# Kernel optimization log

Hardware: AMD Instinct MI355X
Metric: run time of the kernel (lower is better)

The kernel has to match this reference:

```python
import jax, jax.numpy as jnp
import numpy as np

N_NODES = 100000
N_EDGES = 1600000
DIM_NODE = 128
DIM_HID = 128
N_CLASSES = 10


def gcn_conv(x, src, dst, W, b, num_nodes):
    # PyG GCNConv: h = W x; out[i] = sum_j norm_ij * h[j] + b, with self-loops
    # and symmetric normalization norm_ij = deg(i)^-1/2 * deg(j)^-1/2.
    ones = jnp.ones(src.shape[0], dtype=x.dtype)
    deg = jax.ops.segment_sum(ones, dst, num_segments=num_nodes)  # in-degree incl self-loop
    dinv = jnp.where(deg > 0, jax.lax.rsqrt(deg), 0.0)
    norm = dinv[src] * dinv[dst]                                  # [E+N]
    h = x @ W                                                     # [N, out]
    msg = h[src] * norm[:, None]                                  # gather + scale
    out = jax.ops.segment_sum(msg, dst, num_segments=num_nodes)   # scatter-add
    return out + b


def setup_inputs() -> dict:
    key = jax.random.key(0)
    ks = jax.random.split(key, 8)
    x = jax.random.normal(ks[0], (N_NODES, DIM_NODE), dtype=jnp.float32)
    edge_index = jax.random.randint(ks[1], (2, N_EDGES), 0, N_NODES, dtype=jnp.int32)
    def lin(k, fan_in, fan_out):
        s = 1.0 / np.sqrt(fan_in)
        return jax.random.uniform(k, (fan_in, fan_out), jnp.float32, -s, s)
    W1 = lin(ks[2], DIM_NODE, DIM_HID)
    W2 = lin(ks[3], DIM_HID, DIM_HID)
    W3 = lin(ks[4], DIM_HID, DIM_HID)
    fW1 = lin(ks[5], DIM_HID, DIM_HID)
    fW2 = lin(ks[6], DIM_HID, N_CLASSES)
    z = lambda n: jnp.zeros((n,), jnp.float32)
    return {"x": x, "edge_index": edge_index,
            "W1": W1, "b1": z(DIM_HID), "W2": W2, "b2": z(DIM_HID),
            "W3": W3, "b3": z(DIM_HID), "fW1": fW1, "fb1": z(DIM_HID),
            "fW2": fW2, "fb2": z(N_CLASSES)}


def reference(x, edge_index, W1, b1, W2, b2, W3, b3, fW1, fb1, fW2, fb2):
    num_nodes = x.shape[0]
    loop = jnp.arange(num_nodes, dtype=edge_index.dtype)
    src = jnp.concatenate([edge_index[0], loop])  # add self-loops once
    dst = jnp.concatenate([edge_index[1], loop])
    h = jax.nn.relu(gcn_conv(x, src, dst, W1, b1, num_nodes))
    h = jax.nn.relu(gcn_conv(h, src, dst, W2, b2, num_nodes))
    h = jax.nn.relu(gcn_conv(h, src, dst, W3, b3, num_nodes))
    # FFN head (Dropout is identity in eval mode)
    h = jax.nn.relu(h @ fW1 + fb1)
    out = h @ fW2 + fb2
    return out
```

## Files before the change

kernel.cpp:

```cpp
#include <hip/hip_runtime.h>
#include <hip/hip_bf16.h>
#include <hip/hip_fp16.h>

#define DIM 128
#define ROWS 16
#define NCAP 64
#define NSH  6
#define NXCD 8

typedef __attribute__((ext_vector_type(8))) short bf16x8;
typedef __attribute__((ext_vector_type(4))) float f32x4;
typedef _Float16 half_t;

union Frag { unsigned int u[4]; bf16x8 v; uint4 q; };
union H8   { uint4 q; half_t h[8]; };

__device__ __forceinline__ void cvt_hilo(const float* __restrict__ x, Frag& hi, Frag& lo) {
#pragma unroll
    for (int p = 0; p < 4; ++p) {
        float x0 = x[2 * p], x1 = x[2 * p + 1];
        unsigned int h0 = (__float_as_uint(x0) + 0x8000u) & 0xffff0000u;
        unsigned int h1 = (__float_as_uint(x1) + 0x8000u) & 0xffff0000u;
        hi.u[p] = (h0 >> 16) | h1;
        float d0 = x0 - __uint_as_float(h0);
        float d1 = x1 - __uint_as_float(h1);
        lo.u[p] = (__float_as_uint(d0) >> 16) | (__float_as_uint(d1) & 0xffff0000u);
    }
}

__global__ __launch_bounds__(256) void ncur_init_kernel(int* __restrict__ ncur, int N) {
    int n = blockIdx.x * 256 + threadIdx.x;
    if (n < N) ncur[n] = n << NSH;
}

__global__ __launch_bounds__(256) void scatter8_kernel(
    const int* __restrict__ src, const int* __restrict__ dst,
    int* __restrict__ ncur, int* __restrict__ colidx, int E, int N) {
    const int g    = blockIdx.x & (NXCD - 1);
    const int sub  = blockIdx.x >> 3;
    const int nsub = gridDim.x >> 3;
    const int slice = (N + NXCD - 1) / NXCD;
    const int lo = g * slice;
    const int hi = min(lo + slice, N);
    for (int e = sub * 256 + threadIdx.x; e < E; e += nsub * 256) {
        int d = dst[e];
        if (d >= lo && d < hi) {
            int p = atomicAdd(&ncur[d], 1);
            if (p < (d << NSH) + NCAP) colidx[p] = src[e];
        }
    }
}

__global__ __launch_bounds__(256) void ninfo_kernel(
    const int* __restrict__ ncur, unsigned int* __restrict__ ninfo,
    float* __restrict__ dinv, int N) {
    int n = blockIdx.x * 256 + threadIdx.x;
    if (n < N) {
        int deg = min(ncur[n] - (n << NSH), NCAP);
        ninfo[n] = (unsigned int)(n << NSH) | ((unsigned int)deg << 23);
        dinv[n]  = rsqrtf((float)(deg + 1));
    }
}

__global__ __launch_bounds__(256) void wconv_all_kernel(
    const float* __restrict__ W0, const float* __restrict__ W1,
    const float* __restrict__ W2, const float* __restrict__ W3,
    uint4* __restrict__ WFhi, uint4* __restrict__ WFlo) {
    int t  = blockIdx.x * 256 + threadIdx.x;
    int wi = t >> 11;
    const float* W = (wi == 0) ? W0 : (wi == 1) ? W1 : (wi == 2) ? W2 : W3;
    int tt   = t & 2047;
    int lane = tt & 63;
    int f    = tt >> 6;
    int kc   = f >> 3;
    int wc   = (f >> 2) & 1;
    int ct   = f & 3;
    int m    = lane & 15;
    int quad = lane >> 4;
    int col  = wc * 64 + ct * 16 + m;
    int k0   = kc * 32 + quad * 8;
    float wv8[8];
#pragma unroll
    for (int j = 0; j < 8; ++j) wv8[j] = W[(size_t)(k0 + j) * DIM + col];
    Frag hi, lo;
    cvt_hilo(wv8, hi, lo);
    WFhi[t] = hi.q;
    WFlo[t] = lo.q;
}

template<bool GATHER, bool FFN>
__global__ __launch_bounds__(256, 4) void fused16(
    const unsigned int* __restrict__ ninfo, const int* __restrict__ colidx,
    const void* __restrict__ HinV, const float* __restrict__ bg,
    const float* __restrict__ dinv,
    const uint4* __restrict__ WFhi, const uint4* __restrict__ WFlo,
    const float* __restrict__ fb1,
    const float* __restrict__ fW2, const float* __restrict__ fb2,
    void* __restrict__ YV, int N)
{
    __shared__ uint4 Sbuf[512];
    __shared__ float Wl[FFN ? (DIM * 10 + 16) : 1];

    const int tid  = threadIdx.x;
    const int row0 = blockIdx.x * ROWS;

    if constexpr (FFN) {
        for (int i = tid; i < DIM * 10; i += 256) Wl[i] = fW2[i];
        if (tid < 10) Wl[DIM * 10 + tid] = fb2[tid];
    }

    {
        const int row  = tid >> 4;
        const int oct  = tid & 15;
        const int node = row0 + row;
        float acc8[8];
        if (node < N) {
            if constexpr (GATHER) {
                const half_t* hb = (const half_t*)HinV + oct * 8;
                H8 sv; sv.q = *(const uint4*)(hb + (size_t)node * DIM);
                float a[8];
#pragma unroll
                for (int j = 0; j < 8; ++j) a[j] = (float)sv.h[j];
                unsigned int info = ninfo[node];
                int beg = (int)(info & 0x7FFFFF);
                int end = beg + (int)(info >> 23);
                int e = beg;
                for (; e + 4 <= end; e += 4) {
                    H8 v0, v1, v2, v3;
                    v0.q = *(const uint4*)(hb + (size_t)colidx[e]     * DIM);
                    v1.q = *(const uint4*)(hb + (size_t)colidx[e + 1] * DIM);
                    v2.q = *(const uint4*)(hb + (size_t)colidx[e + 2] * DIM);
                    v3.q = *(const uint4*)(hb + (size_t)colidx[e + 3] * DIM);
#pragma unroll
                    for (int j = 0; j < 8; ++j)
                        a[j] += ((float)v0.h[j] + (float)v1.h[j]) + ((float)v2.h[j] + (float)v3.h[j]);
                }
                for (; e < end; ++e) {
                    H8 v0; v0.q = *(const uint4*)(hb + (size_t)colidx[e] * DIM);
#pragma unroll
                    for (int j = 0; j < 8; ++j) a[j] += (float)v0.h[j];
                }
                float sc = dinv[node];
                const float* bp = bg + oct * 8;
#pragma unroll
                for (int j = 0; j < 8; ++j)
                    acc8[j] = fmaxf(fmaf(a[j], sc, bp[j]), 0.f);
            } else {
                const float* xp = (const float*)HinV + (size_t)node * DIM + oct * 8;
                float4 a0 = *(const float4*)xp;
                float4 a1 = *(const float4*)(xp + 4);
                acc8[0] = a0.x; acc8[1] = a0.y; acc8[2] = a0.z; acc8[3] = a0.w;
                acc8[4] = a1.x; acc8[5] = a1.y; acc8[6] = a1.z; acc8[7] = a1.w;
            }
        } else {
#pragma unroll
            for (int j = 0; j < 8; ++j) acc8[j] = 0.f;
        }
        Frag hi, lo;
        cvt_hilo(acc8, hi, lo);
        int fi = (oct >> 2) * 64 + (oct & 3) * 16 + (row ^ oct);
        Sbuf[fi]       = hi.q;
        Sbuf[256 + fi] = lo.q;
    }
    __syncthreads();

    const int lane = tid & 63;
    const int w    = tid >> 6;
    const int m    = lane & 15;
    const int quad = lane >> 4;

    f32x4 acc[2];
    acc[0] = f32x4{0.f, 0.f, 0.f, 0.f};
    acc[1] = f32x4{0.f, 0.f, 0.f, 0.f};

#pragma unroll
    for (int kc = 0; kc < 4; ++kc) {
        Frag ahi, alo;
        int fi = kc * 64 + quad * 16 + (m ^ (kc * 4 + quad));
        ahi.q = Sbuf[fi];
        alo.q = Sbuf[256 + fi];
#pragma unroll
        for (int j = 0; j < 2; ++j) {
            int ctg = w * 2 + j;
            Frag bhi, blo;
            int idx = (kc * 8 + ctg) * 64 + lane;
            bhi.q = WFhi[idx];
            blo.q = WFlo[idx];
            acc[j] = __builtin_amdgcn_mfma_f32_16x16x32_bf16(ahi.v, bhi.v, acc[j], 0, 0, 0);
            acc[j] = __builtin_amdgcn_mfma_f32_16x16x32_bf16(ahi.v, blo.v, acc[j], 0, 0, 0);
            acc[j] = __builtin_amdgcn_mfma_f32_16x16x32_bf16(alo.v, bhi.v, acc[j], 0, 0, 0);
        }
    }

    if constexpr (!FFN) {
        half_t* Y = (half_t*)YV;
#pragma unroll
        for (int r = 0; r < 4; ++r) {
            int grow = row0 + quad * 4 + r;
            if (grow >= N) continue;
            float s = dinv[grow];
#pragma unroll
            for (int j = 0; j < 2; ++j)
                Y[(size_t)grow * DIM + w * 32 + j * 16 + m] = (half_t)(acc[j][r] * s);
        }
    } else {
        float* Y = (float*)YV;
        __syncthreads();
        float* hbuf = (float*)Sbuf;
#pragma unroll
        for (int r = 0; r < 4; ++r) {
            int lrow = quad * 4 + r;
#pragma unroll
            for (int j = 0; j < 2; ++j) {
                int col = w * 32 + j * 16 + m;
                hbuf[lrow * DIM + col] = fmaxf(acc[j][r] + fb1[col], 0.f);
            }
        }
        __syncthreads();
        if (tid < ROWS * 10) {
            int r  = tid / 10;
            int cc = tid - r * 10;
            int grow = row0 + r;
            if (grow < N) {
                float a = 0.f;
#pragma unroll 8
                for (int kk = 0; kk < DIM; ++kk) {
                    int k = (kk + r * 4) & 127;
                    a = fmaf(hbuf[r * DIM + k], Wl[k * 10 + cc], a);
                }
                Y[(size_t)grow * 10 + cc] = a + Wl[DIM * 10 + cc];
            }
        }
    }
}

extern "C" void kernel_launch(void* const* d_in, const int* in_sizes, int n_in,
                              void* d_out, int out_size, void* d_ws, size_t ws_size,
                              hipStream_t stream) {
    const float* x   = (const float*)d_in[0];
    const int*   ei  = (const int*)  d_in[1];
    const float* W1  = (const float*)d_in[2];
    const float* b1  = (const float*)d_in[3];
    const float* W2  = (const float*)d_in[4];
    const float* b2  = (const float*)d_in[5];
    const float* W3  = (const float*)d_in[6];
    const float* b3  = (const float*)d_in[7];
    const float* fW1 = (const float*)d_in[8];
    const float* fb1 = (const float*)d_in[9];
    const float* fW2 = (const float*)d_in[10];
    const float* fb2 = (const float*)d_in[11];
    float* out = (float*)d_out;

    const int N = in_sizes[0] / DIM;
    const int E = in_sizes[1] / 2;
    const int* srcI = ei;
    const int* dstI = ei + E;

    char* ws = (char*)d_ws;
    size_t off = 0;
    auto carve = [&](size_t bytes) { void* p = ws + off; off = (off + bytes + 255) & ~(size_t)255; return p; };
    float* dinv       = (float*)carve((size_t)N * 4);
    unsigned int* ninfo = (unsigned int*)carve((size_t)N * 4);
    int*   ncur       = (int*)  carve((size_t)N * 4);
    int*   colidx     = (int*)  carve((size_t)N * NCAP * 4);
    uint4* wfhi       = (uint4*)carve((size_t)4 * 2048 * 16);
    uint4* wflo       = (uint4*)carve((size_t)4 * 2048 * 16);
    half_t* bufA      = (half_t*)carve((size_t)N * DIM * 2);
    half_t* bufB      = (half_t*)carve((size_t)N * DIM * 2);

    dim3 blk(256);
    int gN  = (N + 255) / 256;
    int gG  = (N + ROWS - 1) / ROWS;
    int gSc = 512 * NXCD;

    wconv_all_kernel<<<32, blk, 0, stream>>>(W1, W2, W3, fW1, wfhi, wflo);

    ncur_init_kernel<<<gN, blk, 0, stream>>>(ncur, N);
    scatter8_kernel<<<gSc, blk, 0, stream>>>(srcI, dstI, ncur, colidx, E, N);
    ninfo_kernel<<<gN, blk, 0, stream>>>(ncur, ninfo, dinv, N);

    fused16<false, false><<<gG, blk, 0, stream>>>(nullptr, nullptr, x, nullptr, dinv,
                                                  wfhi + 0 * 2048, wflo + 0 * 2048,
                                                  nullptr, nullptr, nullptr, bufA, N);

    fused16<true, false><<<gG, blk, 0, stream>>>(ninfo, colidx, bufA, b1, dinv,
                                                 wfhi + 1 * 2048, wflo + 1 * 2048,
                                                 nullptr, nullptr, nullptr, bufB, N);

    fused16<true, false><<<gG, blk, 0, stream>>>(ninfo, colidx, bufB, b2, dinv,
                                                 wfhi + 2 * 2048, wflo + 2 * 2048,
                                                 nullptr, nullptr, nullptr, bufA, N);

    fused16<true, true><<<gG, blk, 0, stream>>>(ninfo, colidx, bufA, b3, dinv,
                                                wfhi + 3 * 2048, wflo + 3 * 2048,
                                                fb1, fW2, fb2, out, N);
}
```

Measured before the change: 429.3 us.

## Partition edges into per-slice staging buffers before CSR scatter; drop ninfo pass

Replaces the scatter kernel, in which every slice group re-read all edges, with a two-pass build. The first pass partitions edges into eight destination-slice staging buffers using block-local counts. The second pass does the per-node atomic scatter reading only its own slice. The ninfo/dinv kernel is removed, and degree and normalisation are computed inline from ncur in the fused kernels. The gather loop is also unrolled to 8 neighbours with vectorised int4 colidx loads. The hardcoded SLICE and SCAP values assume N=100000 and a bounded per-slice edge count, and edges beyond SCAP are silently dropped.

```diff
diff --git a/kernel.cpp b/kernel.cpp
--- a/kernel.cpp
+++ b/kernel.cpp
@@ -7,6 +7,8 @@
 #define NCAP 64
 #define NSH  6
 #define NXCD 8
+#define SLICE 12500
+#define SCAP  208896
 
 typedef __attribute__((ext_vector_type(8))) short bf16x8;
 typedef __attribute__((ext_vector_type(4))) float f32x4;
@@ -28,37 +30,51 @@
     }
 }
 
-__global__ __launch_bounds__(256) void ncur_init_kernel(int* __restrict__ ncur, int N) {
+__global__ __launch_bounds__(256) void ncur_init_kernel(int* __restrict__ ncur,
+                                                        int* __restrict__ scur, int N) {
     int n = blockIdx.x * 256 + threadIdx.x;
     if (n < N) ncur[n] = n << NSH;
-}
-
-__global__ __launch_bounds__(256) void scatter8_kernel(
+    if (blockIdx.x == 0 && threadIdx.x < NXCD) scur[threadIdx.x] = 0;
+}
+
+#define ACHUNK 2048
+__global__ __launch_bounds__(256) void edge_part_kernel(
     const int* __restrict__ src, const int* __restrict__ dst,
-    int* __restrict__ ncur, int* __restrict__ colidx, int E, int N) {
+    int* __restrict__ scur, unsigned int* __restrict__ stg, int E) {
+    __shared__ int cnt[NXCD], base[NXCD], pos[NXCD];
+    const int tid = threadIdx.x;
+    const int e0 = blockIdx.x * ACHUNK;
+    const int e1 = min(e0 + ACHUNK, E);
+    if (tid < NXCD) { cnt[tid] = 0; pos[tid] = 0; }
+    __syncthreads();
+    for (int e = e0 + tid; e < e1; e += 256)
+        atomicAdd(&cnt[dst[e] / SLICE], 1);
+    __syncthreads();
+    if (tid < NXCD) base[tid] = atomicAdd(&scur[tid], cnt[tid]);
+    __syncthreads();
+    for (int e = e0 + tid; e < e1; e += 256) {
+        int d = dst[e];
+        int s = d / SLICE;
+        int p = base[s] + atomicAdd(&pos[s], 1);
+        unsigned int v = (unsigned int)src[e] | ((unsigned int)(d - s * SLICE) << 17);
+        if (p < SCAP) stg[(size_t)s * SCAP + p] = v;
+    }
+}
+
+__global__ __launch_bounds__(256) void edge_scatter_kernel(
+    const unsigned int* __restrict__ stg, const int* __restrict__ scur,
+    int* __restrict__ ncur, int* __restrict__ colidx) {
     const int g    = blockIdx.x & (NXCD - 1);
     const int sub  = blockIdx.x >> 3;
     const int nsub = gridDim.x >> 3;
-    const int slice = (N + NXCD - 1) / NXCD;
-    const int lo = g * slice;
-    const int hi = min(lo + slice, N);
-    for (int e = sub * 256 + threadIdx.x; e < E; e += nsub * 256) {
-        int d = dst[e];
-        if (d >= lo && d < hi) {
-            int p = atomicAdd(&ncur[d], 1);
-            if (p < (d << NSH) + NCAP) colidx[p] = src[e];
-        }
-    }
-}
-
-__global__ __launch_bounds__(256) void ninfo_kernel(
-    const int* __restrict__ ncur, unsigned int* __restrict__ ninfo,
-    float* __restrict__ dinv, int N) {
-    int n = blockIdx.x * 256 + threadIdx.x;
-    if (n < N) {
-        int deg = min(ncur[n] - (n << NSH), NCAP);
-        ninfo[n] = (unsigned int)(n << NSH) | ((unsigned int)deg << 23);
-        dinv[n]  = rsqrtf((float)(deg + 1));
+    const int cnt  = min(scur[g], SCAP);
+    const unsigned int* sp = stg + (size_t)g * SCAP;
+    const int nbase = g * SLICE;
+    for (int i = sub * 256 + threadIdx.x; i < cnt; i += nsub * 256) {
+        unsigned int v = sp[i];
+        int d = nbase + (int)(v >> 17);
+        int p = atomicAdd(&ncur[d], 1);
+        if (p < (d << NSH) + NCAP) colidx[p] = (int)(v & 0x1FFFF);
     }
 }
 
@@ -90,9 +106,8 @@
 
 template<bool GATHER, bool FFN>
 __global__ __launch_bounds__(256, 4) void fused16(
-    const unsigned int* __restrict__ ninfo, const int* __restrict__ colidx,
+    const int* __restrict__ ncur, const int* __restrict__ colidx,
     const void* __restrict__ HinV, const float* __restrict__ bg,
-    const float* __restrict__ dinv,
     const uint4* __restrict__ WFhi, const uint4* __restrict__ WFlo,
     const float* __restrict__ fb1,
     const float* __restrict__ fW2, const float* __restrict__ fb2,
@@ -121,26 +136,44 @@
                 float a[8];
 #pragma unroll
                 for (int j = 0; j < 8; ++j) a[j] = (float)sv.h[j];
-                unsigned int info = ninfo[node];
-                int beg = (int)(info & 0x7FFFFF);
-                int end = beg + (int)(info >> 23);
-                int e = beg;
-                for (; e + 4 <= end; e += 4) {
+                const int beg = node << NSH;
+                const int deg = min(ncur[node] - beg, NCAP);
+                int e = 0;
+                for (; e + 8 <= deg; e += 8) {
+                    int4 c0 = *(const int4*)&colidx[beg + e];
+                    int4 c1 = *(const int4*)&colidx[beg + e + 4];
+                    H8 v0, v1, v2, v3, v4, v5, v6, v7;
+                    v0.q = *(const uint4*)(hb + (size_t)c0.x * DIM);
+                    v1.q = *(const uint4*)(hb + (size_t)c0.y * DIM);
+                    v2.q = *(const uint4*)(hb + (size_t)c0.z * DIM);
+                    v3.q = *(const uint4*)(hb + (size_t)c0.w * DIM);
+                    v4.q = *(const uint4*)(hb + (size_t)c1.x * DIM);
+                    v5.q = *(const uint4*)(hb + (size_t)c1.y * DIM);
+                    v6.q = *(const uint4*)(hb + (size_t)c1.z * DIM);
+                    v7.q = *(const uint4*)(hb + (size_t)c1.w * DIM);
+#pragma unroll
+                    for (int j = 0; j < 8; ++j)
+                        a[j] += (((float)v0.h[j] + (float)v1.h[j]) + ((float)v2.h[j] + (float)v3.h[j]))
+                              + (((float)v4.h[j] + (float)v5.h[j]) + ((float)v6.h[j] + (float)v7.h[j]));
+                }
+                if (e + 4 <= deg) {
+                    int4 c0 = *(const int4*)&colidx[beg + e];
                     H8 v0, v1, v2, v3;
-                    v0.q = *(const uint4*)(hb + (size_t)colidx[e]     * DIM);
-                    v1.q = *(const uint4*)(hb + (size_t)colidx[e + 1] * DIM);
-                    v2.q = *(const uint4*)(hb + (size_t)colidx[e + 2] * DIM);
-                    v3.q = *(const uint4*)(hb + (size_t)colidx[e + 3] * DIM);
+                    v0.q = *(const uint4*)(hb + (size_t)c0.x * DIM);
+                    v1.q = *(const uint4*)(hb + (size_t)c0.y * DIM);
+                    v2.q = *(const uint4*)(hb + (size_t)c0.z * DIM);
+                    v3.q = *(const uint4*)(hb + (size_t)c0.w * DIM);
 #pragma unroll
                     for (int j = 0; j < 8; ++j)
                         a[j] += ((float)v0.h[j] + (float)v1.h[j]) + ((float)v2.h[j] + (float)v3.h[j]);
+                    e += 4;
                 }
-                for (; e < end; ++e) {
-                    H8 v0; v0.q = *(const uint4*)(hb + (size_t)colidx[e] * DIM);
+                for (; e < deg; ++e) {
+                    H8 v0; v0.q = *(const uint4*)(hb + (size_t)colidx[beg + e] * DIM);
 #pragma unroll
                     for (int j = 0; j < 8; ++j) a[j] += (float)v0.h[j];
                 }
-                float sc = dinv[node];
+                float sc = rsqrtf((float)(deg + 1));
                 const float* bp = bg + oct * 8;
 #pragma unroll
                 for (int j = 0; j < 8; ++j)
@@ -198,7 +231,8 @@
         for (int r = 0; r < 4; ++r) {
             int grow = row0 + quad * 4 + r;
             if (grow >= N) continue;
-            float s = dinv[grow];
+            int deg = min(ncur[grow] - (grow << NSH), NCAP);
+            float s = rsqrtf((float)(deg + 1));
 #pragma unroll
             for (int j = 0; j < 2; ++j)
                 Y[(size_t)grow * DIM + w * 32 + j * 16 + m] = (half_t)(acc[j][r] * s);
@@ -259,10 +293,10 @@
     char* ws = (char*)d_ws;
     size_t off = 0;
     auto carve = [&](size_t bytes) { void* p = ws + off; off = (off + bytes + 255) & ~(size_t)255; return p; };
-    float* dinv       = (float*)carve((size_t)N * 4);
-    unsigned int* ninfo = (unsigned int*)carve((size_t)N * 4);
     int*   ncur       = (int*)  carve((size_t)N * 4);
+    int*   scur       = (int*)  carve((size_t)NXCD * 4);
     int*   colidx     = (int*)  carve((size_t)N * NCAP * 4);
+    unsigned int* stg = (unsigned int*)carve((size_t)NXCD * SCAP * 4);
     uint4* wfhi       = (uint4*)carve((size_t)4 * 2048 * 16);
     uint4* wflo       = (uint4*)carve((size_t)4 * 2048 * 16);
     half_t* bufA      = (half_t*)carve((size_t)N * DIM * 2);
@@ -271,27 +305,28 @@
     dim3 blk(256);
     int gN  = (N + 255) / 256;
     int gG  = (N + ROWS - 1) / ROWS;
-    int gSc = 512 * NXCD;
+    int gA  = (E + ACHUNK - 1) / ACHUNK;
+    int gB  = 512 * NXCD;
 
     wconv_all_kernel<<<32, blk, 0, stream>>>(W1, W2, W3, fW1, wfhi, wflo);
 
-    ncur_init_kernel<<<gN, blk, 0, stream>>>(ncur, N);
-    scatter8_kernel<<<gSc, blk, 0, stream>>>(srcI, dstI, ncur, colidx, E, N);
-    ninfo_kernel<<<gN, blk, 0, stream>>>(ncur, ninfo, dinv, N);
-
-    fused16<false, false><<<gG, blk, 0, stream>>>(nullptr, nullptr, x, nullptr, dinv,
+    ncur_init_kernel<<<gN, blk, 0, stream>>>(ncur, scur, N);
+    edge_part_kernel<<<gA, blk, 0, stream>>>(srcI, dstI, scur, stg, E);
+    edge_scatter_kernel<<<gB, blk, 0, stream>>>(stg, scur, ncur, colidx);
+
+    fused16<false, false><<<gG, blk, 0, stream>>>(ncur, nullptr, x, nullptr,
                                                   wfhi + 0 * 2048, wflo + 0 * 2048,
                                                   nullptr, nullptr, nullptr, bufA, N);
 
-    fused16<true, false><<<gG, blk, 0, stream>>>(ninfo, colidx, bufA, b1, dinv,
+    fused16<true, false><<<gG, blk, 0, stream>>>(ncur, colidx, bufA, b1,
                                                  wfhi + 1 * 2048, wflo + 1 * 2048,
                                                  nullptr, nullptr, nullptr, bufB, N);
 
-    fused16<true, false><<<gG, blk, 0, stream>>>(ninfo, colidx, bufB, b2, dinv,
+    fused16<true, false><<<gG, blk, 0, stream>>>(ncur, colidx, bufB, b2,
                                                  wfhi + 2 * 2048, wflo + 2 * 2048,
                                                  nullptr, nullptr, nullptr, bufA, N);
 
-    fused16<true, true><<<gG, blk, 0, stream>>>(ninfo, colidx, bufA, b3, dinv,
+    fused16<true, true><<<gG, blk, 0, stream>>>(ncur, colidx, bufA, b3,
                                                 wfhi + 3 * 2048, wflo + 3 * 2048,
                                                 fb1, fW2, fb2, out, N);
 }
```

Result: slower. 451.2 us (+5.1%).

## Overlap CSR scatter with first-layer GEMM in a combined kernel, drop ninfo

Applied to the files above, without the earlier changes.

The edge scatter that builds the adjacency lists now runs inside the same launch as the first-layer X·W GEMM: every fifth block does scatter work and the rest do GEMM tiles, so the atomic-bound scatter can overlap with the matrix work. Because dinv is not yet known when the first GEMM runs, the first gather applies the source-node dinv per neighbour. Weight conversion and ncur init are merged into one init kernel, and ninfo is replaced by reading ncur directly with int4 colidx loads. Launch bounds are raised to 8 blocks per CU. The scatter loses its per-XCD destination partitioning, which may raise cross-die atomic contention, and the first gather does extra dinv loads.

```diff
diff --git a/kernel.cpp b/kernel.cpp
--- a/kernel.cpp
+++ b/kernel.cpp
@@ -6,7 +6,6 @@
 #define ROWS 16
 #define NCAP 64
 #define NSH  6
-#define NXCD 8
 
 typedef __attribute__((ext_vector_type(8))) short bf16x8;
 typedef __attribute__((ext_vector_type(4))) float f32x4;
@@ -28,70 +27,135 @@
     }
 }
 
-__global__ __launch_bounds__(256) void ncur_init_kernel(int* __restrict__ ncur, int N) {
-    int n = blockIdx.x * 256 + threadIdx.x;
-    if (n < N) ncur[n] = n << NSH;
-}
-
-__global__ __launch_bounds__(256) void scatter8_kernel(
-    const int* __restrict__ src, const int* __restrict__ dst,
-    int* __restrict__ ncur, int* __restrict__ colidx, int E, int N) {
-    const int g    = blockIdx.x & (NXCD - 1);
-    const int sub  = blockIdx.x >> 3;
-    const int nsub = gridDim.x >> 3;
-    const int slice = (N + NXCD - 1) / NXCD;
-    const int lo = g * slice;
-    const int hi = min(lo + slice, N);
-    for (int e = sub * 256 + threadIdx.x; e < E; e += nsub * 256) {
-        int d = dst[e];
-        if (d >= lo && d < hi) {
-            int p = atomicAdd(&ncur[d], 1);
-            if (p < (d << NSH) + NCAP) colidx[p] = src[e];
-        }
-    }
-}
-
-__global__ __launch_bounds__(256) void ninfo_kernel(
-    const int* __restrict__ ncur, unsigned int* __restrict__ ninfo,
-    float* __restrict__ dinv, int N) {
+__global__ __launch_bounds__(256) void init_kernel(
+    const float* __restrict__ W0, const float* __restrict__ W1,
+    const float* __restrict__ W2, const float* __restrict__ W3,
+    uint4* __restrict__ WFhi, uint4* __restrict__ WFlo,
+    int* __restrict__ ncur, int N) {
+    int t = blockIdx.x * 256 + threadIdx.x;
+    if (t < 8192) {
+        int wi = t >> 11;
+        const float* W = (wi == 0) ? W0 : (wi == 1) ? W1 : (wi == 2) ? W2 : W3;
+        int tt   = t & 2047;
+        int lane = tt & 63;
+        int f    = tt >> 6;
+        int kc   = f >> 3;
+        int wc   = (f >> 2) & 1;
+        int ct   = f & 3;
+        int m    = lane & 15;
+        int quad = lane >> 4;
+        int col  = wc * 64 + ct * 16 + m;
+        int k0   = kc * 32 + quad * 8;
+        float wv8[8];
+#pragma unroll
+        for (int j = 0; j < 8; ++j) wv8[j] = W[(size_t)(k0 + j) * DIM + col];
+        Frag hi, lo;
+        cvt_hilo(wv8, hi, lo);
+        WFhi[t] = hi.q;
+        WFlo[t] = lo.q;
+    }
+    int n = t - 8192;
+    if (n >= 0 && n < N) ncur[n] = n << NSH;
+}
+
+__global__ __launch_bounds__(256) void dinv_kernel(
+    const int* __restrict__ ncur, float* __restrict__ dinv, int N) {
     int n = blockIdx.x * 256 + threadIdx.x;
     if (n < N) {
         int deg = min(ncur[n] - (n << NSH), NCAP);
-        ninfo[n] = (unsigned int)(n << NSH) | ((unsigned int)deg << 23);
-        dinv[n]  = rsqrtf((float)(deg + 1));
-    }
-}
-
-__global__ __launch_bounds__(256) void wconv_all_kernel(
-    const float* __restrict__ W0, const float* __restrict__ W1,
-    const float* __restrict__ W2, const float* __restrict__ W3,
-    uint4* __restrict__ WFhi, uint4* __restrict__ WFlo) {
-    int t  = blockIdx.x * 256 + threadIdx.x;
-    int wi = t >> 11;
-    const float* W = (wi == 0) ? W0 : (wi == 1) ? W1 : (wi == 2) ? W2 : W3;
-    int tt   = t & 2047;
-    int lane = tt & 63;
-    int f    = tt >> 6;
-    int kc   = f >> 3;
-    int wc   = (f >> 2) & 1;
-    int ct   = f & 3;
-    int m    = lane & 15;
-    int quad = lane >> 4;
-    int col  = wc * 64 + ct * 16 + m;
-    int k0   = kc * 32 + quad * 8;
-    float wv8[8];
-#pragma unroll
-    for (int j = 0; j < 8; ++j) wv8[j] = W[(size_t)(k0 + j) * DIM + col];
-    Frag hi, lo;
-    cvt_hilo(wv8, hi, lo);
-    WFhi[t] = hi.q;
-    WFlo[t] = lo.q;
-}
-
-template<bool GATHER, bool FFN>
-__global__ __launch_bounds__(256, 4) void fused16(
-    const unsigned int* __restrict__ ninfo, const int* __restrict__ colidx,
-    const void* __restrict__ HinV, const float* __restrict__ bg,
+        dinv[n] = rsqrtf((float)(deg + 1));
+    }
+}
+
+__global__ __launch_bounds__(256, 8) void mega_kernel(
+    const float* __restrict__ X,
+    const uint4* __restrict__ WFhi, const uint4* __restrict__ WFlo,
+    half_t* __restrict__ Y,
+    const int* __restrict__ src, const int* __restrict__ dst,
+    int* __restrict__ ncur, int* __restrict__ colidx,
+    int E, int N, int nGemm)
+{
+    __shared__ uint4 Sbuf[512];
+    const int bid = blockIdx.x;
+    const int tid = threadIdx.x;
+
+    if ((bid % 5) == 4) {
+        const int sIdx  = bid / 5;
+        const int nScat = gridDim.x / 5;
+        for (int e = sIdx * 256 + tid; e < E; e += nScat * 256) {
+            int d = dst[e];
+            int p = atomicAdd(&ncur[d], 1);
+            if (p < (d << NSH) + NCAP) colidx[p] = src[e];
+        }
+        return;
+    }
+    const int g = bid - (bid + 1) / 5;
+    if (g >= nGemm) return;
+    const int row0 = g * ROWS;
+
+    {
+        const int row  = tid >> 4;
+        const int oct  = tid & 15;
+        const int node = row0 + row;
+        float acc8[8];
+        if (node < N) {
+            const float* xp = X + (size_t)node * DIM + oct * 8;
+            float4 a0 = *(const float4*)xp;
+            float4 a1 = *(const float4*)(xp + 4);
+            acc8[0] = a0.x; acc8[1] = a0.y; acc8[2] = a0.z; acc8[3] = a0.w;
+            acc8[4] = a1.x; acc8[5] = a1.y; acc8[6] = a1.z; acc8[7] = a1.w;
+        } else {
+#pragma unroll
+            for (int j = 0; j < 8; ++j) acc8[j] = 0.f;
+        }
+        Frag hi, lo;
+        cvt_hilo(acc8, hi, lo);
+        int fi = (oct >> 2) * 64 + (oct & 3) * 16 + (row ^ oct);
+        Sbuf[fi]       = hi.q;
+        Sbuf[256 + fi] = lo.q;
+    }
+    __syncthreads();
+
+    const int lane = tid & 63;
+    const int w    = tid >> 6;
+    const int m    = lane & 15;
+    const int quad = lane >> 4;
+    f32x4 acc[2];
+    acc[0] = f32x4{0.f, 0.f, 0.f, 0.f};
+    acc[1] = f32x4{0.f, 0.f, 0.f, 0.f};
+#pragma unroll
+    for (int kc = 0; kc < 4; ++kc) {
+        Frag ahi, alo;
+        int fi = kc * 64 + quad * 16 + (m ^ (kc * 4 + quad));
+        ahi.q = Sbuf[fi];
+        alo.q = Sbuf[256 + fi];
+#pragma unroll
+        for (int j = 0; j < 2; ++j) {
+            int ctg = w * 2 + j;
+            Frag bhi, blo;
+            int idx = (kc * 8 + ctg) * 64 + lane;
+            bhi.q = WFhi[idx];
+            blo.q = WFlo[idx];
+            acc[j] = __builtin_amdgcn_mfma_f32_16x16x32_bf16(ahi.v, bhi.v, acc[j], 0, 0, 0);
+            acc[j] = __builtin_amdgcn_mfma_f32_16x16x32_bf16(ahi.v, blo.v, acc[j], 0, 0, 0);
+            acc[j] = __builtin_amdgcn_mfma_f32_16x16x32_bf16(alo.v, bhi.v, acc[j], 0, 0, 0);
+        }
+    }
+
+#pragma unroll
+    for (int r = 0; r < 4; ++r) {
+        int grow = row0 + quad * 4 + r;
+        if (grow >= N) continue;
+#pragma unroll
+        for (int j = 0; j < 2; ++j)
+            Y[(size_t)grow * DIM + w * 32 + j * 16 + m] = (half_t)acc[j][r];
+    }
+}
+
+template<bool SRCSCALE, bool FFN>
+__global__ __launch_bounds__(256, 8) void fused16(
+    const int* __restrict__ ncur, const int* __restrict__ colidx,
+    const half_t* __restrict__ Hin, const float* __restrict__ bg,
     const float* __restrict__ dinv,
     const uint4* __restrict__ WFhi, const uint4* __restrict__ WFlo,
     const float* __restrict__ fb1,
@@ -115,43 +179,53 @@
         const int node = row0 + row;
         float acc8[8];
         if (node < N) {
-            if constexpr (GATHER) {
-                const half_t* hb = (const half_t*)HinV + oct * 8;
-                H8 sv; sv.q = *(const uint4*)(hb + (size_t)node * DIM);
-                float a[8];
-#pragma unroll
-                for (int j = 0; j < 8; ++j) a[j] = (float)sv.h[j];
-                unsigned int info = ninfo[node];
-                int beg = (int)(info & 0x7FFFFF);
-                int end = beg + (int)(info >> 23);
-                int e = beg;
-                for (; e + 4 <= end; e += 4) {
-                    H8 v0, v1, v2, v3;
-                    v0.q = *(const uint4*)(hb + (size_t)colidx[e]     * DIM);
-                    v1.q = *(const uint4*)(hb + (size_t)colidx[e + 1] * DIM);
-                    v2.q = *(const uint4*)(hb + (size_t)colidx[e + 2] * DIM);
-                    v3.q = *(const uint4*)(hb + (size_t)colidx[e + 3] * DIM);
+            const half_t* hb = Hin + oct * 8;
+            H8 sv; sv.q = *(const uint4*)(hb + (size_t)node * DIM);
+            const float dvd = dinv[node];
+            float a[8];
+#pragma unroll
+            for (int j = 0; j < 8; ++j)
+                a[j] = SRCSCALE ? dvd * (float)sv.h[j] : (float)sv.h[j];
+            const int beg = node << NSH;
+            const int deg = min(ncur[node] - beg, NCAP);
+            int e = 0;
+            for (; e + 4 <= deg; e += 4) {
+                int4 c = *(const int4*)&colidx[beg + e];
+                H8 v0, v1, v2, v3;
+                v0.q = *(const uint4*)(hb + (size_t)c.x * DIM);
+                v1.q = *(const uint4*)(hb + (size_t)c.y * DIM);
+                v2.q = *(const uint4*)(hb + (size_t)c.z * DIM);
+                v3.q = *(const uint4*)(hb + (size_t)c.w * DIM);
+                if constexpr (SRCSCALE) {
+                    float d0 = dinv[c.x], d1 = dinv[c.y], d2 = dinv[c.z], d3 = dinv[c.w];
+#pragma unroll
+                    for (int j = 0; j < 8; ++j)
+                        a[j] = fmaf(d3, (float)v3.h[j],
+                               fmaf(d2, (float)v2.h[j],
+                               fmaf(d1, (float)v1.h[j],
+                               fmaf(d0, (float)v0.h[j], a[j]))));
+                } else {
 #pragma unroll
                     for (int j = 0; j < 8; ++j)
                         a[j] += ((float)v0.h[j] + (float)v1.h[j]) + ((float)v2.h[j] + (float)v3.h[j]);
                 }
-                for (; e < end; ++e) {
-                    H8 v0; v0.q = *(const uint4*)(hb + (size_t)colidx[e] * DIM);
+            }
+            for (; e < deg; ++e) {
+                int c = colidx[beg + e];
+                H8 v0; v0.q = *(const uint4*)(hb + (size_t)c * DIM);
+                if constexpr (SRCSCALE) {
+                    float d0 = dinv[c];
+#pragma unroll
+                    for (int j = 0; j < 8; ++j) a[j] = fmaf(d0, (float)v0.h[j], a[j]);
+                } else {
 #pragma unroll
                     for (int j = 0; j < 8; ++j) a[j] += (float)v0.h[j];
                 }
-                float sc = dinv[node];
-                const float* bp = bg + oct * 8;
-#pragma unroll
-                for (int j = 0; j < 8; ++j)
-                    acc8[j] = fmaxf(fmaf(a[j], sc, bp[j]), 0.f);
-            } else {
-                const float* xp = (const float*)HinV + (size_t)node * DIM + oct * 8;
-                float4 a0 = *(const float4*)xp;
-                float4 a1 = *(const float4*)(xp + 4);
-                acc8[0] = a0.x; acc8[1] = a0.y; acc8[2] = a0.z; acc8[3] = a0.w;
-                acc8[4] = a1.x; acc8[5] = a1.y; acc8[6] = a1.z; acc8[7] = a1.w;
             }
+            const float* bp = bg + oct * 8;
+#pragma unroll
+            for (int j = 0; j < 8; ++j)
+                acc8[j] = fmaxf(fmaf(a[j], dvd, bp[j]), 0.f);
         } else {
 #pragma unroll
             for (int j = 0; j < 8; ++j) acc8[j] = 0.f;
@@ -259,9 +333,8 @@
     char* ws = (char*)d_ws;
     size_t off = 0;
     auto carve = [&](size_t bytes) { void* p = ws + off; off = (off + bytes + 255) & ~(size_t)255; return p; };
+    int*   ncur       = (int*)  carve((size_t)N * 4);
     float* dinv       = (float*)carve((size_t)N * 4);
-    unsigned int* ninfo = (unsigned int*)carve((size_t)N * 4);
-    int*   ncur       = (int*)  carve((size_t)N * 4);
     int*   colidx     = (int*)  carve((size_t)N * NCAP * 4);
     uint4* wfhi       = (uint4*)carve((size_t)4 * 2048 * 16);
     uint4* wflo       = (uint4*)carve((size_t)4 * 2048 * 16);
@@ -269,29 +342,27 @@
     half_t* bufB      = (half_t*)carve((size_t)N * DIM * 2);
 
     dim3 blk(256);
-    int gN  = (N + 255) / 256;
-    int gG  = (N + ROWS - 1) / ROWS;
-    int gSc = 512 * NXCD;
-
-    wconv_all_kernel<<<32, blk, 0, stream>>>(W1, W2, W3, fW1, wfhi, wflo);
-
-    ncur_init_kernel<<<gN, blk, 0, stream>>>(ncur, N);
-    scatter8_kernel<<<gSc, blk, 0, stream>>>(srcI, dstI, ncur, colidx, E, N);
-    ninfo_kernel<<<gN, blk, 0, stream>>>(ncur, ninfo, dinv, N);
-
-    fused16<false, false><<<gG, blk, 0, stream>>>(nullptr, nullptr, x, nullptr, dinv,
-                                                  wfhi + 0 * 2048, wflo + 0 * 2048,
-                                                  nullptr, nullptr, nullptr, bufA, N);
-
-    fused16<true, false><<<gG, blk, 0, stream>>>(ninfo, colidx, bufA, b1, dinv,
-                                                 wfhi + 1 * 2048, wflo + 1 * 2048,
-                                                 nullptr, nullptr, nullptr, bufB, N);
-
-    fused16<true, false><<<gG, blk, 0, stream>>>(ninfo, colidx, bufB, b2, dinv,
-                                                 wfhi + 2 * 2048, wflo + 2 * 2048,
-                                                 nullptr, nullptr, nullptr, bufA, N);
-
-    fused16<true, true><<<gG, blk, 0, stream>>>(ninfo, colidx, bufA, b3, dinv,
-                                                wfhi + 3 * 2048, wflo + 3 * 2048,
-                                                fb1, fW2, fb2, out, N);
-}
+    int nGemm = (N + ROWS - 1) / ROWS;
+    int gInit = (8192 + N + 255) / 256;
+    int gN    = (N + 255) / 256;
+    int gMega = (nGemm * 5 + 3) / 4;
+
+    init_kernel<<<gInit, blk, 0, stream>>>(W1, W2, W3, fW1, wfhi, wflo, ncur, N);
+
+    mega_kernel<<<gMega, blk, 0, stream>>>(x, wfhi + 0 * 2048, wflo + 0 * 2048, bufA,
+                                           srcI, dstI, ncur, colidx, E, N, nGemm);
+
+    dinv_kernel<<<gN, blk, 0, stream>>>(ncur, dinv, N);
+
+    fused16<true, false><<<nGemm, blk, 0, stream>>>(ncur, colidx, bufA, b1, dinv,
+                                                    wfhi + 1 * 2048, wflo + 1 * 2048,
+                                                    nullptr, nullptr, nullptr, bufB, N);
+
+    fused16<false, false><<<nGemm, blk, 0, stream>>>(ncur, colidx, bufB, b2, dinv,
+                                                     wfhi + 2 * 2048, wflo + 2 * 2048,
+                                                     nullptr, nullptr, nullptr, bufA, N);
+
+    fused16<false, true><<<nGemm, blk, 0, stream>>>(ncur, colidx, bufA, b3, dinv,
+                                                    wfhi + 3 * 2048, wflo + 3 * 2048,
+                                                    fb1, fW2, fb2, out, N);
+}
```

Result: no change. 425.9 us (-0.8%).
